# Optimization experiments

Measured on AMD Instinct MI355X. Metric: run time of the kernel, lower is better.

Reference implementation:

```python
import jax, jax.numpy as jnp
import numpy as np

B, T, D, H, F = 2, 2048, 2048, 16, 8192
DH = D // H  # 128
EPS = 1e-6   # flax LayerNorm default


def _layernorm(x, scale, bias):
    mu = jnp.mean(x, axis=-1, keepdims=True)
    var = jnp.mean(jnp.square(x - mu), axis=-1, keepdims=True)
    return (x - mu) * jax.lax.rsqrt(var + EPS) * scale + bias


def setup_inputs() -> dict:
    key = jax.random.key(0)
    ks = jax.random.split(key, 8)
    w = 0.02
    return {
        "x": jax.random.normal(ks[0], (B, T, D), jnp.float32),
        "ln1_scale": jnp.ones((D,), jnp.float32),
        "ln1_bias": jnp.zeros((D,), jnp.float32),
        "w_qkv": jax.random.normal(ks[1], (D, 3 * D), jnp.float32) * w,
        "b_qkv": jnp.zeros((3 * D,), jnp.float32),
        "ln2_scale": jnp.ones((D,), jnp.float32),
        "ln2_bias": jnp.zeros((D,), jnp.float32),
        "w1": jax.random.normal(ks[2], (D, F), jnp.float32) * w,
        "b1": jnp.zeros((F,), jnp.float32),
        "w2": jax.random.normal(ks[3], (F, D), jnp.float32) * w,
        "b2": jnp.zeros((D,), jnp.float32),
    }


def reference(x, ln1_scale, ln1_bias, w_qkv, b_qkv, ln2_scale, ln2_bias, w1, b1, w2, b2):
    # --- pre-LN causal self-attention (training=False -> dropout = identity) ---
    r = _layernorm(x, ln1_scale, ln1_bias)
    qkv = r @ w_qkv + b_qkv                       # [B,T,3D]
    q, k, v = jnp.split(qkv, 3, axis=-1)
    q = q.reshape(B, T, H, DH)
    k = k.reshape(B, T, H, DH)
    v = v.reshape(B, T, H, DH)
    attn = jnp.einsum('bthd,bThd->bhtT', q, k) / jnp.sqrt(jnp.float32(DH))
    causal = jnp.tril(jnp.ones((T, T), bool))
    attn = jnp.where(causal, attn, -jnp.inf)
    attn = jax.nn.softmax(attn, axis=-1)
    out = jnp.einsum('bhtT,bThd->bthd', attn, v).reshape(B, T, D)
    # NOTE: original module has no output projection after attention.
    x = x + out
    # --- MLP block ---
    r = _layernorm(x, ln2_scale, ln2_bias)
    h = jax.nn.gelu(r @ w1 + b1, approximate=True)  # flax nn.gelu default
    x = x + (h @ w2 + b2)
    return x
```

## Files before the change

kernel.cpp:

```cpp
#include <hip/hip_runtime.h>
#include <hip/hip_bf16.h>
#include <stdint.h>
#include <stddef.h>

using bf16_t = __hip_bfloat16;
typedef __attribute__((ext_vector_type(8))) short short8;
typedef __attribute__((ext_vector_type(4))) short short4v;
typedef __attribute__((ext_vector_type(4))) float f32x4;

__device__ __forceinline__ void gload_lds16(const void* g, void* l) {
  __builtin_amdgcn_global_load_lds((const __attribute__((address_space(1))) void*)g,
                                   (__attribute__((address_space(3))) void*)l,
                                   16, 0, 0);
}

__global__ __launch_bounds__(256) void k_transpose_cvt(const float* __restrict__ in,
                                                       bf16_t* __restrict__ out,
                                                       int K, int N) {
  __shared__ float tile[64][65];
  int n0 = blockIdx.x * 64, k0 = blockIdx.y * 64;
  int t = threadIdx.x;
  int tr = t >> 4, tc = t & 15;
#pragma unroll
  for (int i = 0; i < 4; ++i) {
    float4 v = *(const float4*)(in + (size_t)(k0 + tr + i * 16) * N + n0 + tc * 4);
    tile[tr + i * 16][tc * 4 + 0] = v.x;
    tile[tr + i * 16][tc * 4 + 1] = v.y;
    tile[tr + i * 16][tc * 4 + 2] = v.z;
    tile[tr + i * 16][tc * 4 + 3] = v.w;
  }
  __syncthreads();
#pragma unroll
  for (int i = 0; i < 4; ++i) {
    int nn = tr + i * 16;
    short4v s;
    s[0] = (short)__bfloat16_as_ushort(__float2bfloat16(tile[tc * 4 + 0][nn]));
    s[1] = (short)__bfloat16_as_ushort(__float2bfloat16(tile[tc * 4 + 1][nn]));
    s[2] = (short)__bfloat16_as_ushort(__float2bfloat16(tile[tc * 4 + 2][nn]));
    s[3] = (short)__bfloat16_as_ushort(__float2bfloat16(tile[tc * 4 + 3][nn]));
    *(short4v*)(out + (size_t)(n0 + nn) * K + k0 + tc * 4) = s;
  }
}

__global__ __launch_bounds__(256) void k_layernorm(const float* __restrict__ x,
                                                   const float* __restrict__ gam,
                                                   const float* __restrict__ bet,
                                                   bf16_t* __restrict__ out) {
  int row = blockIdx.x, t = threadIdx.x;
  const float4* xr = (const float4*)(x + (size_t)row * 2048);
  float4 a = xr[t], b = xr[t + 256];
  float s  = a.x + a.y + a.z + a.w + b.x + b.y + b.z + b.w;
  float s2 = a.x*a.x + a.y*a.y + a.z*a.z + a.w*a.w
           + b.x*b.x + b.y*b.y + b.z*b.z + b.w*b.w;
#pragma unroll
  for (int off = 32; off >= 1; off >>= 1) {
    s  += __shfl_xor(s, off);
    s2 += __shfl_xor(s2, off);
  }
  __shared__ float red[8];
  if ((t & 63) == 0) { red[t >> 6] = s; red[4 + (t >> 6)] = s2; }
  __syncthreads();
  float S  = red[0] + red[1] + red[2] + red[3];
  float S2 = red[4] + red[5] + red[6] + red[7];
  float mu = S * (1.0f / 2048.0f);
  float var = S2 * (1.0f / 2048.0f) - mu * mu;
  float rstd = rsqrtf(var + 1e-6f);
  const float4* gv = (const float4*)gam;
  const float4* bv = (const float4*)bet;
  float4 g1 = gv[t], g2 = gv[t + 256], c1 = bv[t], c2 = bv[t + 256];
  bf16_t* orow = out + (size_t)row * 2048;
  orow[4*t + 0]    = __float2bfloat16((a.x - mu) * rstd * g1.x + c1.x);
  orow[4*t + 1]    = __float2bfloat16((a.y - mu) * rstd * g1.y + c1.y);
  orow[4*t + 2]    = __float2bfloat16((a.z - mu) * rstd * g1.z + c1.z);
  orow[4*t + 3]    = __float2bfloat16((a.w - mu) * rstd * g1.w + c1.w);
  orow[1024 + 4*t + 0] = __float2bfloat16((b.x - mu) * rstd * g2.x + c2.x);
  orow[1024 + 4*t + 1] = __float2bfloat16((b.y - mu) * rstd * g2.y + c2.y);
  orow[1024 + 4*t + 2] = __float2bfloat16((b.z - mu) * rstd * g2.z + c2.z);
  orow[1024 + 4*t + 3] = __float2bfloat16((b.w - mu) * rstd * g2.w + c2.w);
}

template <int EPI>
__global__ __launch_bounds__(512, 2) void k_gemm8(const bf16_t* __restrict__ A,
                                                  const bf16_t* __restrict__ Bt,
                                                  const float* __restrict__ bias,
                                                  bf16_t* __restrict__ Cb,
                                                  float* __restrict__ Cf,
                                                  int Ndim, int LDA, int LDB,
                                                  int Kdim, int nsub) {
  __shared__ __align__(16) char lds[131072];
  int orig = blockIdx.x;
  int xcd = orig & 7;
  int i = orig >> 3;
  int m = i & 15;
  int j = i >> 4;
  int n_local = j % nsub;
  int chunk = j / nsub;
  int m0 = m * 256;
  int n0 = (xcd * nsub + n_local) * 256;
  int tid = threadIdx.x;
  int w = tid >> 6, lane = tid & 63;
  int lr = lane & 15, lk = lane >> 4;
  int wr = w >> 2, wc = w & 3;

  const bf16_t* Ag = A + (size_t)m0 * LDA + (size_t)chunk * Kdim;
  const bf16_t* Bg = Bt + (size_t)n0 * LDB + (size_t)chunk * Kdim;
  int swch = ((tid & 7) ^ ((tid >> 3) & 7)) << 3;
  const bf16_t* pA0 = Ag + (size_t)(tid >> 3) * LDA + swch;
  const bf16_t* pA1 = pA0 + (size_t)128 * LDA;
  int nb0 = ((tid >> 8) & 1) * 64 + ((tid >> 3) & 31);
  const bf16_t* pB0 = Bg + (size_t)nb0 * LDB + swch;
  const bf16_t* pB1 = pB0 + (size_t)128 * LDB;
  int dstb = tid * 16;
  int chv0 = ((lk)     ^ (lr & 7)) * 16;
  int chv1 = ((4 + lk) ^ (lr & 7)) * 16;
  int aof0 = 65536 + wr * 8192 + lr * 128 + chv0;
  int aof1 = 65536 + wr * 8192 + lr * 128 + chv1;
  int bof0 = wc * 4096 + lr * 128 + chv0;
  int bof1 = wc * 4096 + lr * 128 + chv1;

  f32x4 acc[8][4];
#pragma unroll
  for (int ii = 0; ii < 8; ++ii)
#pragma unroll
    for (int jj = 0; jj < 4; ++jj) acc[ii][jj] = (f32x4){0.f, 0.f, 0.f, 0.f};
  short8 af[4][2], bq[2][2];

#define STAGE_A(p, h, kt) do { \
    size_t ko = (size_t)(kt) * 64 + (size_t)(h) * 64 * LDA; \
    gload_lds16(pA0 + ko, lds + 65536 + (p) * 32768 + (h) * 16384 + dstb); \
    gload_lds16(pA1 + ko, lds + 65536 + (p) * 32768 + (h) * 16384 + 8192 + dstb); } while (0)
#define STAGE_B(p, h, kt) do { \
    size_t ko = (size_t)(kt) * 64 + (size_t)(h) * 32 * LDB; \
    gload_lds16(pB0 + ko, lds + (p) * 32768 + (h) * 16384 + dstb); \
    gload_lds16(pB1 + ko, lds + (p) * 32768 + (h) * 16384 + 8192 + dstb); } while (0)
#define READ_A(p, mh) do { \
    _Pragma("unroll") for (int mf = 0; mf < 4; ++mf) { \
      af[mf][0] = *(const short8*)(lds + (p) * 32768 + (mh) * 16384 + mf * 2048 + aof0); \
      af[mf][1] = *(const short8*)(lds + (p) * 32768 + (mh) * 16384 + mf * 2048 + aof1); } } while (0)
#define READ_B(p, nh) do { \
    _Pragma("unroll") for (int nf = 0; nf < 2; ++nf) { \
      bq[nf][0] = *(const short8*)(lds + (p) * 32768 + (nh) * 16384 + nf * 2048 + bof0); \
      bq[nf][1] = *(const short8*)(lds + (p) * 32768 + (nh) * 16384 + nf * 2048 + bof1); } } while (0)
#define MM16(mh, nh) do { \
    _Pragma("unroll") for (int ks = 0; ks < 2; ++ks) \
    _Pragma("unroll") for (int mf = 0; mf < 4; ++mf) \
    _Pragma("unroll") for (int nf = 0; nf < 2; ++nf) \
      acc[(mh) * 4 + mf][(nh) * 2 + nf] = __builtin_amdgcn_mfma_f32_16x16x32_bf16( \
          af[mf][ks], bq[nf][ks], acc[(mh) * 4 + mf][(nh) * 2 + nf], 0, 0, 0); } while (0)
#define BARRIER() asm volatile("s_barrier" ::: "memory")
#define LGKM0()  do { asm volatile("s_waitcnt lgkmcnt(0)" ::: "memory"); __builtin_amdgcn_sched_barrier(0); } while (0)
#define PRIO1()  __builtin_amdgcn_s_setprio(1)
#define PRIO0()  __builtin_amdgcn_s_setprio(0)
#define BODY(t, p, S1, S2, VMN) do { \
    READ_A(p, 0); READ_B(p, 0); \
    if (S1) STAGE_B((p) ^ 1, 0, (t) + 1); \
    asm volatile("s_waitcnt lgkmcnt(8)" ::: "memory"); \
    BARRIER(); LGKM0(); PRIO1(); MM16(0, 0); PRIO0(); BARRIER(); \
    READ_B(p, 1); \
    if (S2) STAGE_A(p, 0, (t) + 2); \
    BARRIER(); LGKM0(); PRIO1(); MM16(0, 1); PRIO0(); BARRIER(); \
    READ_A(p, 1); \
    if (S2) STAGE_B(p, 1, (t) + 2); \
    BARRIER(); LGKM0(); PRIO1(); MM16(1, 1); PRIO0(); BARRIER(); \
    READ_B(p, 0); \
    if (S2) STAGE_A(p, 1, (t) + 2); \
    BARRIER(); LGKM0(); PRIO1(); MM16(1, 0); PRIO0(); \
    asm volatile("s_waitcnt vmcnt(%0)" :: "i"(VMN) : "memory"); \
    BARRIER(); } while (0)

  const int NT = Kdim >> 6;
  STAGE_A(0, 0, 0); STAGE_B(0, 0, 0); STAGE_B(0, 1, 0); STAGE_A(0, 1, 0);
  STAGE_A(1, 0, 1); STAGE_B(1, 1, 1); STAGE_A(1, 1, 1);
  asm volatile("s_waitcnt vmcnt(6)" ::: "memory");
  BARRIER();

  int t = 0;
  for (; t + 3 < NT; t += 2) {
    BODY(t, 0, 1, 1, 6);
    BODY(t + 1, 1, 1, 1, 6);
  }
  BODY(t, 0, 1, 0, 0);
  {
    READ_A(1, 0); READ_B(1, 0);
    BARRIER(); LGKM0(); MM16(0, 0); BARRIER();
    READ_B(1, 1);
    BARRIER(); LGKM0(); MM16(0, 1); BARRIER();
    READ_A(1, 1);
    BARRIER(); LGKM0(); MM16(1, 1); BARRIER();
    READ_B(1, 0);
    LGKM0(); MM16(1, 0);
  }
#undef STAGE_A
#undef STAGE_B
#undef READ_A
#undef READ_B
#undef MM16
#undef BARRIER
#undef LGKM0
#undef PRIO1
#undef PRIO0
#undef BODY

#pragma unroll
  for (int mf = 0; mf < 8; ++mf) {
#pragma unroll
    for (int nf = 0; nf < 4; ++nf) {
#pragma unroll
      for (int r = 0; r < 4; ++r) {
        int rw = m0 + wr * 128 + mf * 16 + lk * 4 + r;
        int cl = n0 + wc * 64 + nf * 16 + lr;
        float v = acc[mf][nf][r];
        size_t gi = (size_t)rw * Ndim + cl;
        if (EPI == 0) {
          Cb[gi] = __float2bfloat16(v + bias[cl]);
        } else if (EPI == 1) {
          float vv = v + bias[cl];
          float u = vv * (vv * vv * 0.044715f + 1.0f) * 0.7978845608028654f;
          float gl = 0.5f * vv * (1.0f + tanhf(u));
          Cb[gi] = __float2bfloat16(gl);
        } else {
          float add = v + (chunk == 0 ? bias[cl] : 0.0f);
          atomicAdd(&Cf[gi], add);
        }
      }
    }
  }
}

__global__ __launch_bounds__(256) void k_transpose_v(const bf16_t* __restrict__ qkv,
                                                     bf16_t* __restrict__ vT) {
  __shared__ bf16_t tile[64][72];
  int bid = blockIdx.x;
  int tt = bid & 31;
  int dt = (bid >> 5) & 1;
  int h  = (bid >> 6) & 15;
  int b  = bid >> 10;
  int t0 = tt * 64, d0 = dt * 64;
  int t = threadIdx.x;
  const bf16_t* src = qkv + (size_t)(b * 2048) * 6144 + 4096 + h * 128;
#pragma unroll
  for (int i = 0; i < 16; ++i) {
    int idx = t + i * 256;
    int rr = idx >> 6, cc = idx & 63;
    tile[rr][cc] = src[(size_t)(t0 + rr) * 6144 + d0 + cc];
  }
  __syncthreads();
  bf16_t* dst = vT + (size_t)(b * 16 + h) * 128 * 2048;
#pragma unroll
  for (int i = 0; i < 16; ++i) {
    int idx = t + i * 256;
    int rr = idx >> 6, cc = idx & 63;
    dst[(size_t)(d0 + rr) * 2048 + t0 + cc] = tile[cc][rr];
  }
}

__global__ __launch_bounds__(256, 2) void k_attn(const bf16_t* __restrict__ qkv,
                                                 const bf16_t* __restrict__ vT,
                                                 const float* __restrict__ x,
                                                 float* __restrict__ out) {
  __shared__ __align__(16) bf16_t Pl[4][32][40];
  int j = blockIdx.x;
  int bh = j & 31;
  int cq = j >> 5;
  int b = bh >> 4, h = bh & 15;
  int w = threadIdx.x >> 6, lane = threadIdx.x & 63;
  int lr = lane & 15, lk = lane >> 4;
  int c = (w == 0) ? cq : (w == 1) ? (63 - cq) : (w == 2) ? (31 - cq) : (32 + cq);
  int q0 = c * 32;
  const bf16_t* qb = qkv + (size_t)(b * 2048) * 6144 + h * 128;
  const bf16_t* kb = qb + 2048;
  const bf16_t* vb = vT + (size_t)(b * 16 + h) * 128 * 2048;
  short8 qf[2][4];
#pragma unroll
  for (int qg = 0; qg < 2; ++qg)
#pragma unroll
    for (int d4 = 0; d4 < 4; ++d4)
      qf[qg][d4] = *(const short8*)(qb + (size_t)(q0 + qg * 16 + lr) * 6144 + d4 * 32 + lk * 8);
  float m[2][4], l[2][4];
#pragma unroll
  for (int qg = 0; qg < 2; ++qg)
#pragma unroll
    for (int r = 0; r < 4; ++r) { m[qg][r] = -1e30f; l[qg][r] = 0.f; }
  f32x4 o[2][8] = {};
  int nkt = c + 1;
  const float sc = 0.08838834764831845f;
  short8 kf[2][4], vf[8];
#pragma unroll
  for (int nt = 0; nt < 2; ++nt)
#pragma unroll
    for (int d4 = 0; d4 < 4; ++d4)
      kf[nt][d4] = *(const short8*)(kb + (size_t)(nt * 16 + lr) * 6144 + d4 * 32 + lk * 8);
#pragma unroll
  for (int d8 = 0; d8 < 8; ++d8)
    vf[d8] = *(const short8*)(vb + (size_t)(d8 * 16 + lr) * 2048 + lk * 8);

  for (int kt = 0; kt < nkt; ++kt) {
    int tk0 = kt * 32;
    f32x4 s[2][2] = {};
    __builtin_amdgcn_s_setprio(1);
#pragma unroll
    for (int d4 = 0; d4 < 4; ++d4)
#pragma unroll
      for (int qg = 0; qg < 2; ++qg)
#pragma unroll
        for (int nt = 0; nt < 2; ++nt)
          s[qg][nt] = __builtin_amdgcn_mfma_f32_16x16x32_bf16(qf[qg][d4], kf[nt][d4], s[qg][nt], 0, 0, 0);
    __builtin_amdgcn_s_setprio(0);
    if (kt + 1 < nkt) {
      int tn = tk0 + 32;
#pragma unroll
      for (int nt = 0; nt < 2; ++nt)
#pragma unroll
        for (int d4 = 0; d4 < 4; ++d4)
          kf[nt][d4] = *(const short8*)(kb + (size_t)(tn + nt * 16 + lr) * 6144 + d4 * 32 + lk * 8);
    }
#pragma unroll
    for (int qg = 0; qg < 2; ++qg) {
      float sv[2][4], mt[4];
#pragma unroll
      for (int r = 0; r < 4; ++r) {
        int qr = q0 + qg * 16 + lk * 4 + r;
#pragma unroll
        for (int nt = 0; nt < 2; ++nt) {
          float v = s[qg][nt][r] * sc;
          int kc = tk0 + nt * 16 + lr;
          sv[nt][r] = (kc > qr) ? -1e30f : v;
        }
        mt[r] = fmaxf(sv[0][r], sv[1][r]);
      }
#pragma unroll
      for (int off = 1; off < 16; off <<= 1)
#pragma unroll
        for (int r = 0; r < 4; ++r) mt[r] = fmaxf(mt[r], __shfl_xor(mt[r], off));
      float alpha[4], rs[4];
#pragma unroll
      for (int r = 0; r < 4; ++r) {
        float mn = fmaxf(m[qg][r], mt[r]);
        alpha[r] = __expf(m[qg][r] - mn);
        m[qg][r] = mn;
      }
#pragma unroll
      for (int r = 0; r < 4; ++r) {
        float p0 = __expf(sv[0][r] - m[qg][r]);
        float p1 = __expf(sv[1][r] - m[qg][r]);
        rs[r] = p0 + p1;
        Pl[w][qg * 16 + lk * 4 + r][lr]      = __float2bfloat16(p0);
        Pl[w][qg * 16 + lk * 4 + r][16 + lr] = __float2bfloat16(p1);
      }
#pragma unroll
      for (int off = 1; off < 16; off <<= 1)
#pragma unroll
        for (int r = 0; r < 4; ++r) rs[r] += __shfl_xor(rs[r], off);
#pragma unroll
      for (int r = 0; r < 4; ++r) l[qg][r] = l[qg][r] * alpha[r] + rs[r];
#pragma unroll
      for (int d8 = 0; d8 < 8; ++d8)
#pragma unroll
        for (int r = 0; r < 4; ++r) o[qg][d8][r] *= alpha[r];
    }
    asm volatile("s_waitcnt lgkmcnt(0)" ::: "memory");
    short8 pf[2];
#pragma unroll
    for (int qg = 0; qg < 2; ++qg)
      pf[qg] = *(const short8*)(&Pl[w][qg * 16 + lr][lk * 8]);
    __builtin_amdgcn_s_setprio(1);
#pragma unroll
    for (int d8 = 0; d8 < 8; ++d8)
#pragma unroll
      for (int qg = 0; qg < 2; ++qg)
        o[qg][d8] = __builtin_amdgcn_mfma_f32_16x16x32_bf16(pf[qg], vf[d8], o[qg][d8], 0, 0, 0);
    __builtin_amdgcn_s_setprio(0);
    if (kt + 1 < nkt) {
      int tn = tk0 + 32;
#pragma unroll
      for (int d8 = 0; d8 < 8; ++d8)
        vf[d8] = *(const short8*)(vb + (size_t)(d8 * 16 + lr) * 2048 + tn + lk * 8);
    }
  }
#pragma unroll
  for (int qg = 0; qg < 2; ++qg)
#pragma unroll
    for (int d8 = 0; d8 < 8; ++d8)
#pragma unroll
      for (int r = 0; r < 4; ++r) {
        int qr = q0 + qg * 16 + lk * 4 + r;
        int cl = h * 128 + d8 * 16 + lr;
        size_t gi = (size_t)(b * 2048 + qr) * 2048 + cl;
        out[gi] = x[gi] + o[qg][d8][r] / l[qg][r];
      }
}

extern "C" void kernel_launch(void* const* d_in, const int* in_sizes, int n_in,
                              void* d_out, int out_size, void* d_ws, size_t ws_size,
                              hipStream_t stream) {
  const float* x    = (const float*)d_in[0];
  const float* ln1s = (const float*)d_in[1];
  const float* ln1b = (const float*)d_in[2];
  const float* wqkv = (const float*)d_in[3];
  const float* bqkv = (const float*)d_in[4];
  const float* ln2s = (const float*)d_in[5];
  const float* ln2b = (const float*)d_in[6];
  const float* w1   = (const float*)d_in[7];
  const float* b1   = (const float*)d_in[8];
  const float* w2   = (const float*)d_in[9];
  const float* b2   = (const float*)d_in[10];
  float* out = (float*)d_out;
  char* ws = (char*)d_ws;

  bf16_t* r     = (bf16_t*)(ws + 0);
  bf16_t* vT    = (bf16_t*)(ws + 0);
  bf16_t* qkv   = (bf16_t*)(ws + 16777216);
  bf16_t* w1T   = (bf16_t*)(ws + 67108864);
  bf16_t* w2T   = (bf16_t*)(ws + 100663296);
  bf16_t* h     = (bf16_t*)(ws + 134217728);
  bf16_t* wqkvT = (bf16_t*)(ws + 134217728);

  k_transpose_cvt<<<dim3(96, 32),  256, 0, stream>>>(wqkv, wqkvT, 2048, 6144);
  k_transpose_cvt<<<dim3(128, 32), 256, 0, stream>>>(w1,   w1T,   2048, 8192);
  k_transpose_cvt<<<dim3(32, 128), 256, 0, stream>>>(w2,   w2T,   8192, 2048);
  k_layernorm<<<4096, 256, 0, stream>>>(x, ln1s, ln1b, r);
  k_gemm8<0><<<384, 512, 0, stream>>>(r, wqkvT, bqkv, qkv, nullptr, 6144, 2048, 2048, 2048, 3);
  k_transpose_v<<<2048, 256, 0, stream>>>(qkv, vT);
  k_attn<<<512, 256, 0, stream>>>(qkv, vT, x, out);
  k_layernorm<<<4096, 256, 0, stream>>>(out, ln2s, ln2b, r);
  k_gemm8<1><<<512, 512, 0, stream>>>(r, w1T, b1, h, nullptr, 8192, 2048, 2048, 2048, 4);
  k_gemm8<3><<<256, 512, 0, stream>>>(h, w2T, b2, nullptr, out, 2048, 8192, 8192, 4096, 1);
}
```

Measured before the change: 656.4 us.

## Fuse V transpose into QKV GEMM epilogue and keep both B fragment halves in registers

The QKV GEMM gets a new epilogue mode that writes the V columns directly into the transposed per-head layout. This removes the separate transpose kernel and its round trip through memory. Separately, the GEMM mainloop keeps both halves of the B fragments in separate register sets, which drops one LDS re-read and one lgkm wait per k-step. The cost is extra VGPR pressure under 2-wave occupancy bounds, plus 8-byte scattered stores for V, which could hurt coalescing.

```diff
diff --git a/kernel.cpp b/kernel.cpp
--- a/kernel.cpp
+++ b/kernel.cpp
@@ -85,6 +85,7 @@
                                                   const float* __restrict__ bias,
                                                   bf16_t* __restrict__ Cb,
                                                   float* __restrict__ Cf,
+                                                  bf16_t* __restrict__ Vt,
                                                   int Ndim, int LDA, int LDB,
                                                   int Kdim, int nsub) {
   __shared__ __align__(16) char lds[131072];
@@ -123,7 +124,7 @@
   for (int ii = 0; ii < 8; ++ii)
 #pragma unroll
     for (int jj = 0; jj < 4; ++jj) acc[ii][jj] = (f32x4){0.f, 0.f, 0.f, 0.f};
-  short8 af[4][2], bq[2][2];
+  short8 af[4][2], bq0[2][2], bq1[2][2];
 
 #define STAGE_A(p, h, kt) do { \
     size_t ko = (size_t)(kt) * 64 + (size_t)(h) * 64 * LDA; \
@@ -137,34 +138,38 @@
     _Pragma("unroll") for (int mf = 0; mf < 4; ++mf) { \
       af[mf][0] = *(const short8*)(lds + (p) * 32768 + (mh) * 16384 + mf * 2048 + aof0); \
       af[mf][1] = *(const short8*)(lds + (p) * 32768 + (mh) * 16384 + mf * 2048 + aof1); } } while (0)
-#define READ_B(p, nh) do { \
+#define READ_B0(p) do { \
     _Pragma("unroll") for (int nf = 0; nf < 2; ++nf) { \
-      bq[nf][0] = *(const short8*)(lds + (p) * 32768 + (nh) * 16384 + nf * 2048 + bof0); \
-      bq[nf][1] = *(const short8*)(lds + (p) * 32768 + (nh) * 16384 + nf * 2048 + bof1); } } while (0)
+      bq0[nf][0] = *(const short8*)(lds + (p) * 32768 + nf * 2048 + bof0); \
+      bq0[nf][1] = *(const short8*)(lds + (p) * 32768 + nf * 2048 + bof1); } } while (0)
+#define READ_B1(p) do { \
+    _Pragma("unroll") for (int nf = 0; nf < 2; ++nf) { \
+      bq1[nf][0] = *(const short8*)(lds + (p) * 32768 + 16384 + nf * 2048 + bof0); \
+      bq1[nf][1] = *(const short8*)(lds + (p) * 32768 + 16384 + nf * 2048 + bof1); } } while (0)
 #define MM16(mh, nh) do { \
     _Pragma("unroll") for (int ks = 0; ks < 2; ++ks) \
     _Pragma("unroll") for (int mf = 0; mf < 4; ++mf) \
     _Pragma("unroll") for (int nf = 0; nf < 2; ++nf) \
       acc[(mh) * 4 + mf][(nh) * 2 + nf] = __builtin_amdgcn_mfma_f32_16x16x32_bf16( \
-          af[mf][ks], bq[nf][ks], acc[(mh) * 4 + mf][(nh) * 2 + nf], 0, 0, 0); } while (0)
+          af[mf][ks], (nh) ? bq1[nf][ks] : bq0[nf][ks], \
+          acc[(mh) * 4 + mf][(nh) * 2 + nf], 0, 0, 0); } while (0)
 #define BARRIER() asm volatile("s_barrier" ::: "memory")
 #define LGKM0()  do { asm volatile("s_waitcnt lgkmcnt(0)" ::: "memory"); __builtin_amdgcn_sched_barrier(0); } while (0)
 #define PRIO1()  __builtin_amdgcn_s_setprio(1)
 #define PRIO0()  __builtin_amdgcn_s_setprio(0)
 #define BODY(t, p, S1, S2, VMN) do { \
-    READ_A(p, 0); READ_B(p, 0); \
+    READ_A(p, 0); READ_B0(p); \
     if (S1) STAGE_B((p) ^ 1, 0, (t) + 1); \
     asm volatile("s_waitcnt lgkmcnt(8)" ::: "memory"); \
     BARRIER(); LGKM0(); PRIO1(); MM16(0, 0); PRIO0(); BARRIER(); \
-    READ_B(p, 1); \
+    READ_B1(p); \
     if (S2) STAGE_A(p, 0, (t) + 2); \
     BARRIER(); LGKM0(); PRIO1(); MM16(0, 1); PRIO0(); BARRIER(); \
     READ_A(p, 1); \
     if (S2) STAGE_B(p, 1, (t) + 2); \
     BARRIER(); LGKM0(); PRIO1(); MM16(1, 1); PRIO0(); BARRIER(); \
-    READ_B(p, 0); \
     if (S2) STAGE_A(p, 1, (t) + 2); \
-    BARRIER(); LGKM0(); PRIO1(); MM16(1, 0); PRIO0(); \
+    BARRIER(); PRIO1(); MM16(1, 0); PRIO0(); \
     asm volatile("s_waitcnt vmcnt(%0)" :: "i"(VMN) : "memory"); \
     BARRIER(); } while (0)
 
@@ -181,19 +186,19 @@
   }
   BODY(t, 0, 1, 0, 0);
   {
-    READ_A(1, 0); READ_B(1, 0);
+    READ_A(1, 0); READ_B0(1);
     BARRIER(); LGKM0(); MM16(0, 0); BARRIER();
-    READ_B(1, 1);
+    READ_B1(1);
     BARRIER(); LGKM0(); MM16(0, 1); BARRIER();
     READ_A(1, 1);
     BARRIER(); LGKM0(); MM16(1, 1); BARRIER();
-    READ_B(1, 0);
-    LGKM0(); MM16(1, 0);
+    MM16(1, 0);
   }
 #undef STAGE_A
 #undef STAGE_B
 #undef READ_A
-#undef READ_B
+#undef READ_B0
+#undef READ_B1
 #undef MM16
 #undef BARRIER
 #undef LGKM0
@@ -201,6 +206,26 @@
 #undef PRIO0
 #undef BODY
 
+  if (EPI == 4 && n0 >= 4096) {
+#pragma unroll
+    for (int mf = 0; mf < 8; ++mf) {
+#pragma unroll
+      for (int nf = 0; nf < 4; ++nf) {
+        int cl = n0 + wc * 64 + nf * 16 + lr;
+        int d = cl - 4096;
+        int hh = d >> 7, dh = d & 127;
+        int rwb = m0 + wr * 128 + mf * 16 + lk * 4;
+        int bb = rwb >> 11, tt = rwb & 2047;
+        float bs = bias[cl];
+        short4v s;
+#pragma unroll
+        for (int r = 0; r < 4; ++r)
+          s[r] = (short)__bfloat16_as_ushort(__float2bfloat16(acc[mf][nf][r] + bs));
+        *(short4v*)(Vt + ((size_t)(bb * 16 + hh) * 128 + dh) * 2048 + tt) = s;
+      }
+    }
+    return;
+  }
 #pragma unroll
   for (int mf = 0; mf < 8; ++mf) {
 #pragma unroll
@@ -211,7 +236,7 @@
         int cl = n0 + wc * 64 + nf * 16 + lr;
         float v = acc[mf][nf][r];
         size_t gi = (size_t)rw * Ndim + cl;
-        if (EPI == 0) {
+        if (EPI == 0 || EPI == 4) {
           Cb[gi] = __float2bfloat16(v + bias[cl]);
         } else if (EPI == 1) {
           float vv = v + bias[cl];
@@ -224,33 +249,6 @@
         }
       }
     }
-  }
-}
-
-__global__ __launch_bounds__(256) void k_transpose_v(const bf16_t* __restrict__ qkv,
-                                                     bf16_t* __restrict__ vT) {
-  __shared__ bf16_t tile[64][72];
-  int bid = blockIdx.x;
-  int tt = bid & 31;
-  int dt = (bid >> 5) & 1;
-  int h  = (bid >> 6) & 15;
-  int b  = bid >> 10;
-  int t0 = tt * 64, d0 = dt * 64;
-  int t = threadIdx.x;
-  const bf16_t* src = qkv + (size_t)(b * 2048) * 6144 + 4096 + h * 128;
-#pragma unroll
-  for (int i = 0; i < 16; ++i) {
-    int idx = t + i * 256;
-    int rr = idx >> 6, cc = idx & 63;
-    tile[rr][cc] = src[(size_t)(t0 + rr) * 6144 + d0 + cc];
-  }
-  __syncthreads();
-  bf16_t* dst = vT + (size_t)(b * 16 + h) * 128 * 2048;
-#pragma unroll
-  for (int i = 0; i < 16; ++i) {
-    int idx = t + i * 256;
-    int rr = idx >> 6, cc = idx & 63;
-    dst[(size_t)(d0 + rr) * 2048 + t0 + cc] = tile[cc][rr];
   }
 }
 
@@ -408,21 +406,20 @@
   char* ws = (char*)d_ws;
 
   bf16_t* r     = (bf16_t*)(ws + 0);
-  bf16_t* vT    = (bf16_t*)(ws + 0);
   bf16_t* qkv   = (bf16_t*)(ws + 16777216);
   bf16_t* w1T   = (bf16_t*)(ws + 67108864);
   bf16_t* w2T   = (bf16_t*)(ws + 100663296);
   bf16_t* h     = (bf16_t*)(ws + 134217728);
   bf16_t* wqkvT = (bf16_t*)(ws + 134217728);
+  bf16_t* vT    = (bf16_t*)(ws + 167772160);
 
   k_transpose_cvt<<<dim3(96, 32),  256, 0, stream>>>(wqkv, wqkvT, 2048, 6144);
   k_transpose_cvt<<<dim3(128, 32), 256, 0, stream>>>(w1,   w1T,   2048, 8192);
   k_transpose_cvt<<<dim3(32, 128), 256, 0, stream>>>(w2,   w2T,   8192, 2048);
   k_layernorm<<<4096, 256, 0, stream>>>(x, ln1s, ln1b, r);
-  k_gemm8<0><<<384, 512, 0, stream>>>(r, wqkvT, bqkv, qkv, nullptr, 6144, 2048, 2048, 2048, 3);
-  k_transpose_v<<<2048, 256, 0, stream>>>(qkv, vT);
+  k_gemm8<4><<<384, 512, 0, stream>>>(r, wqkvT, bqkv, qkv, nullptr, vT, 6144, 2048, 2048, 2048, 3);
   k_attn<<<512, 256, 0, stream>>>(qkv, vT, x, out);
   k_layernorm<<<4096, 256, 0, stream>>>(out, ln2s, ln2b, r);
-  k_gemm8<1><<<512, 512, 0, stream>>>(r, w1T, b1, h, nullptr, 8192, 2048, 2048, 2048, 4);
-  k_gemm8<3><<<256, 512, 0, stream>>>(h, w2T, b2, nullptr, out, 2048, 8192, 8192, 4096, 1);
-}
+  k_gemm8<1><<<512, 512, 0, stream>>>(r, w1T, b1, h, nullptr, nullptr, 8192, 2048, 2048, 2048, 4);
+  k_gemm8<3><<<256, 512, 0, stream>>>(h, w2T, b2, nullptr, out, nullptr, 2048, 8192, 8192, 4096, 1);
+}
```

Result: no change. 648.5 us, median of 2 (-1.2%).
